# Performance work log

Hardware: AMD Instinct MI355X
Metric: run time of the kernel (lower is better)

The kernel has to match this reference:

```python
import jax, jax.numpy as jnp
import numpy as np

DEPTH = 10
B, F = 8192, 512
NUM_INTERNAL = 2 ** DEPTH - 1   # 1023
NUM_LEAVES = 2 ** DEPTH         # 1024
LEAF_DIMS = 64


def setup_inputs() -> dict:
    key = jax.random.key(0)
    k1, k2, k3 = jax.random.split(key, 3)
    x = jax.random.normal(k1, (B, F), dtype=jnp.float32)
    # All internal-node Dense(1) gates batched into one weight matrix [F, num_internal].
    W = jax.random.normal(k2, (F, NUM_INTERNAL), dtype=jnp.float32) * (1.0 / np.sqrt(F))
    b = jnp.zeros((NUM_INTERNAL,), dtype=jnp.float32)
    leaves_weights = jax.random.normal(k3, (NUM_LEAVES, LEAF_DIMS), dtype=jnp.float32)
    return {"x": x, "W": W, "b": b, "leaves_weights": leaves_weights}


def reference(x, W, b, leaves_weights):
    # All gate probabilities in one fused matmul + sigmoid: [B, num_internal].
    # Node i's gate is column i (BFS / level order, same as the original list of Dense layers).
    p = jax.nn.sigmoid(x @ W + b)
    batch = x.shape[0]
    # Level-by-level probability propagation. prob has shape [B, 2^lvl]:
    # the path probability of each node at the current level.
    prob = jnp.ones((batch, 1), dtype=x.dtype)
    for lvl in range(DEPTH):
        start = 2 ** lvl - 1                      # first node index at this level
        p_lvl = p[:, start:start + 2 ** lvl]      # [B, 2^lvl] gate probs at this level
        # left child gets p * prob, right child gets (1-p) * prob, interleaved in node order
        prob = jnp.stack([p_lvl * prob, (1.0 - p_lvl) * prob], axis=-1)
        prob = prob.reshape(batch, 2 ** (lvl + 1))
    # Leaf-weighted sum: sum_l prob[:, l] * leaves_weights[l, :] -> [B, leaf_dims]
    return prob @ leaves_weights
```

## Files before the change

### kernel.cpp

```cpp
#include <hip/hip_runtime.h>


typedef short bf16x8 __attribute__((ext_vector_type(8)));
typedef float f32x4 __attribute__((ext_vector_type(4)));

#define GLOAD16(g, l) __builtin_amdgcn_global_load_lds( \
    (const __attribute__((address_space(1))) void*)(g), \
    (__attribute__((address_space(3))) void*)(l), 16, 0, 0)

__device__ __forceinline__ unsigned short f2bf(float f) {
    unsigned u = __float_as_uint(f);
    return (unsigned short)((u + 0x7FFFu + ((u >> 16) & 1u)) >> 16);
}

__global__ __launch_bounds__(256) void convert_split(const float* __restrict__ x,
                                                     const float* __restrict__ W,
                                                     unsigned short* __restrict__ xh,
                                                     unsigned short* __restrict__ xl,
                                                     unsigned short* __restrict__ wh,
                                                     unsigned short* __restrict__ wl)
{
    __shared__ float tile[32][33];
    const int b = blockIdx.x;
    const int tid = threadIdx.x;
    if (b < 1024) {
        const float4* xs = reinterpret_cast<const float4*>(x);
        #pragma unroll
        for (int i = 0; i < 4; ++i) {
            const int idx = b * 1024 + i * 256 + tid;
            const float4 v = xs[idx];
            ushort4 h, l;
            h.x = f2bf(v.x); l.x = f2bf(v.x - __uint_as_float((unsigned)h.x << 16));
            h.y = f2bf(v.y); l.y = f2bf(v.y - __uint_as_float((unsigned)h.y << 16));
            h.z = f2bf(v.z); l.z = f2bf(v.z - __uint_as_float((unsigned)h.z << 16));
            h.w = f2bf(v.w); l.w = f2bf(v.w - __uint_as_float((unsigned)h.w << 16));
            reinterpret_cast<ushort4*>(xh)[idx] = h;
            reinterpret_cast<ushort4*>(xl)[idx] = l;
        }
    } else {
        const int tb = b - 1024;
        const int k0 = (tb >> 5) * 32;
        const int n0 = (tb & 31) * 32;
        const int tk = tid >> 5, tn = tid & 31;
        #pragma unroll
        for (int j = 0; j < 4; ++j) {
            const int k = k0 + tk + j * 8;
            const int n = n0 + tn;
            tile[tk + j * 8][tn] = (n < 1023) ? W[(size_t)k * 1023 + n] : 0.f;
        }
        __syncthreads();
        const int wn = tid >> 5, wk = tid & 31;
        #pragma unroll
        for (int j = 0; j < 4; ++j) {
            const int n = n0 + wn + j * 8;
            const float v = tile[wk][wn + j * 8];
            const unsigned short h = f2bf(v);
            const unsigned short lo = f2bf(v - __uint_as_float((unsigned)h << 16));
            wh[(size_t)n * 512 + k0 + wk] = h;
            wl[(size_t)n * 512 + k0 + wk] = lo;
        }
    }
}

__global__ __launch_bounds__(256, 2) void gemm_sig_mfma(
    const unsigned short* __restrict__ xh, const unsigned short* __restrict__ xl,
    const unsigned short* __restrict__ wh, const unsigned short* __restrict__ wl,
    const float* __restrict__ bias, float* __restrict__ p)
{
    __shared__ __align__(16) unsigned short Ah[2][128 * 32];
    __shared__ __align__(16) unsigned short Al[2][128 * 32];
    __shared__ __align__(16) unsigned short Bh[2][128 * 32];
    __shared__ __align__(16) unsigned short Bl[2][128 * 32];

    const int tid = threadIdx.x;
    const int lane = tid & 63;
    const int wv = tid >> 6;
    const int m_base = blockIdx.y * 128;
    const int n_base = blockIdx.x * 128;
    const int wr = wv >> 1, wc = wv & 1;

    f32x4 acc[4][4];
    #pragma unroll
    for (int i = 0; i < 4; ++i)
        #pragma unroll
        for (int j = 0; j < 4; ++j)
            acc[i][j] = (f32x4){0.f, 0.f, 0.f, 0.f};

    const int c0 = tid, c1 = tid + 256;
    const int lb0 = wv * 512;
    const int lb1 = 2048 + wv * 512;
    const int a0row = c0 >> 2, a0kc = (c0 & 3) * 8;
    const int a1row = c1 >> 2, a1kc = (c1 & 3) * 8;
    const int l15 = lane & 15, kg = lane >> 4;

    const size_t ga0 = (size_t)(m_base + a0row) * 512 + a0kc;
    const size_t ga1 = (size_t)(m_base + a1row) * 512 + a1kc;
    const size_t gb0 = (size_t)(n_base + a0row) * 512 + a0kc;
    const size_t gb1 = (size_t)(n_base + a1row) * 512 + a1kc;

    #define STAGE(buf, k0) do { \
        GLOAD16(xh + ga0 + (k0), &Ah[buf][lb0]); \
        GLOAD16(xh + ga1 + (k0), &Ah[buf][lb1]); \
        GLOAD16(xl + ga0 + (k0), &Al[buf][lb0]); \
        GLOAD16(xl + ga1 + (k0), &Al[buf][lb1]); \
        GLOAD16(wh + gb0 + (k0), &Bh[buf][lb0]); \
        GLOAD16(wh + gb1 + (k0), &Bh[buf][lb1]); \
        GLOAD16(wl + gb0 + (k0), &Bl[buf][lb0]); \
        GLOAD16(wl + gb1 + (k0), &Bl[buf][lb1]); \
    } while (0)

    STAGE(0, 0);
    __syncthreads();

    #pragma unroll
    for (int t = 0; t < 16; ++t) {
        const int cur = t & 1;
        if (t < 15) STAGE(cur ^ 1, (t + 1) * 32);

        bf16x8 ah[4], al[4], bh[4], bl[4];
        #pragma unroll
        for (int mi = 0; mi < 4; ++mi) {
            const int off = (wr * 64 + mi * 16 + l15) * 32 + kg * 8;
            ah[mi] = *reinterpret_cast<const bf16x8*>(&Ah[cur][off]);
            al[mi] = *reinterpret_cast<const bf16x8*>(&Al[cur][off]);
        }
        #pragma unroll
        for (int ni = 0; ni < 4; ++ni) {
            const int off = (wc * 64 + ni * 16 + l15) * 32 + kg * 8;
            bh[ni] = *reinterpret_cast<const bf16x8*>(&Bh[cur][off]);
            bl[ni] = *reinterpret_cast<const bf16x8*>(&Bl[cur][off]);
        }
        #pragma unroll
        for (int mi = 0; mi < 4; ++mi)
            #pragma unroll
            for (int ni = 0; ni < 4; ++ni) {
                acc[mi][ni] = __builtin_amdgcn_mfma_f32_16x16x32_bf16(ah[mi], bh[ni], acc[mi][ni], 0, 0, 0);
                acc[mi][ni] = __builtin_amdgcn_mfma_f32_16x16x32_bf16(ah[mi], bl[ni], acc[mi][ni], 0, 0, 0);
                acc[mi][ni] = __builtin_amdgcn_mfma_f32_16x16x32_bf16(al[mi], bh[ni], acc[mi][ni], 0, 0, 0);
            }
        __syncthreads();
    }
    #undef STAGE

    const int l4 = lane >> 4;
    #pragma unroll
    for (int ni = 0; ni < 4; ++ni) {
        const int n = n_base + wc * 64 + ni * 16 + l15;
        if (n < 1023) {
            const float bv = bias[n];
            #pragma unroll
            for (int mi = 0; mi < 4; ++mi) {
                #pragma unroll
                for (int r = 0; r < 4; ++r) {
                    const int m = m_base + wr * 64 + mi * 16 + l4 * 4 + r;
                    const float v = acc[mi][ni][r] + bv;
                    p[(size_t)m * 1024 + 1 + n] = 1.f / (1.f + __expf(-v));
                }
            }
        }
    }
}

__global__ __launch_bounds__(256, 4) void gemm_sig_f32(const float* __restrict__ x,
                                                       const float* __restrict__ W,
                                                       const float* __restrict__ bias,
                                                       float* __restrict__ p)
{
    __shared__ __align__(16) float As[16][128 + 4];
    __shared__ __align__(16) float Bs[16][64 + 4];
    const int tid = threadIdx.x;
    const int m_base = blockIdx.y * 128;
    const int n_base = blockIdx.x * 64;
    const int m0 = (tid >> 4) * 8, n0 = (tid & 15) * 4;
    float acc[8][4];
    #pragma unroll
    for (int i = 0; i < 8; ++i)
        #pragma unroll
        for (int j = 0; j < 4; ++j) acc[i][j] = 0.f;
    const int arow = tid >> 2, acol = (tid & 3) * 4;
    const int bk = tid >> 4, bn = (tid & 15) * 4;
    for (int k0 = 0; k0 < 512; k0 += 16) {
        #pragma unroll
        for (int i = 0; i < 2; ++i) {
            const int row = arow + i * 64;
            const float4 a = *reinterpret_cast<const float4*>(&x[(size_t)(m_base + row) * 512 + k0 + acol]);
            As[0][(acol + 0) * 132 + row] = a.x;
            As[0][(acol + 1) * 132 + row] = a.y;
            As[0][(acol + 2) * 132 + row] = a.z;
            As[0][(acol + 3) * 132 + row] = a.w;
        }
        {
            const int gk = k0 + bk;
            #pragma unroll
            for (int j = 0; j < 4; ++j) {
                const int gn = n_base + bn + j;
                Bs[bk][bn + j] = (gn < 1023) ? W[(size_t)gk * 1023 + gn] : 0.f;
            }
        }
        __syncthreads();
        #pragma unroll
        for (int kk = 0; kk < 16; ++kk) {
            const float4 b4 = *reinterpret_cast<const float4*>(&Bs[kk][n0]);
            const float4 a0 = *reinterpret_cast<const float4*>(&As[kk][m0]);
            const float4 a1 = *reinterpret_cast<const float4*>(&As[kk][m0 + 4]);
            const float a[8] = {a0.x, a0.y, a0.z, a0.w, a1.x, a1.y, a1.z, a1.w};
            const float b[4] = {b4.x, b4.y, b4.z, b4.w};
            #pragma unroll
            for (int i = 0; i < 8; ++i)
                #pragma unroll
                for (int j = 0; j < 4; ++j)
                    acc[i][j] = fmaf(a[i], b[j], acc[i][j]);
        }
        __syncthreads();
    }
    #pragma unroll
    for (int i = 0; i < 8; ++i) {
        const int gm = m_base + m0 + i;
        #pragma unroll
        for (int j = 0; j < 4; ++j) {
            const int gn = n_base + n0 + j;
            if (gn < 1023) {
                float v = acc[i][j] + bias[gn];
                p[(size_t)gm * 1024 + 1 + gn] = 1.0f / (1.0f + __expf(-v));
            }
        }
    }
}

__global__ __launch_bounds__(256, 4) void tree_leaves(const float* __restrict__ p,
                                                      const float* __restrict__ leaves,
                                                      float* __restrict__ out)
{
    __shared__ __align__(16) float prob[8][1024];

    const int tid = threadIdx.x;
    const int row_base = blockIdx.x * 8;
    const int r = tid >> 5, s = tid & 31;
    const float* pr = p + (size_t)(row_base + r) * 1024;

    float prefix = 1.f;
    #pragma unroll
    for (int lvl = 0; lvl < 5; ++lvl) {
        const float v = pr[(1 << lvl) + (s >> (5 - lvl))];
        prefix *= ((s >> (4 - lvl)) & 1) ? (1.f - v) : v;
    }

    float q1[2], q2[4], q3[8], q4[16], q5[32];
    {
        const float v = pr[32 + s];
        q1[0] = prefix * v; q1[1] = prefix * (1.f - v);
    }
    {
        const float2 v2 = *reinterpret_cast<const float2*>(&pr[64 + 2 * s]);
        q2[0] = q1[0] * v2.x; q2[1] = q1[0] * (1.f - v2.x);
        q2[2] = q1[1] * v2.y; q2[3] = q1[1] * (1.f - v2.y);
    }
    {
        const float4 v4 = *reinterpret_cast<const float4*>(&pr[128 + 4 * s]);
        const float v[4] = {v4.x, v4.y, v4.z, v4.w};
        #pragma unroll
        for (int j = 0; j < 4; ++j) {
            q3[2 * j] = q2[j] * v[j]; q3[2 * j + 1] = q2[j] * (1.f - v[j]);
        }
    }
    {
        const float4 va = *reinterpret_cast<const float4*>(&pr[256 + 8 * s]);
        const float4 vb = *reinterpret_cast<const float4*>(&pr[260 + 8 * s]);
        const float v[8] = {va.x, va.y, va.z, va.w, vb.x, vb.y, vb.z, vb.w};
        #pragma unroll
        for (int j = 0; j < 8; ++j) {
            q4[2 * j] = q3[j] * v[j]; q4[2 * j + 1] = q3[j] * (1.f - v[j]);
        }
    }
    {
        float v[16];
        #pragma unroll
        for (int u = 0; u < 4; ++u) {
            const float4 vv = *reinterpret_cast<const float4*>(&pr[512 + 16 * s + 4 * u]);
            v[4 * u] = vv.x; v[4 * u + 1] = vv.y; v[4 * u + 2] = vv.z; v[4 * u + 3] = vv.w;
        }
        #pragma unroll
        for (int j = 0; j < 16; ++j) {
            q5[2 * j] = q4[j] * v[j]; q5[2 * j + 1] = q4[j] * (1.f - v[j]);
        }
    }

    const int sw = (s & 7) << 2;
    #pragma unroll
    for (int u = 0; u < 32; u += 4) {
        float4 q; q.x = q5[u]; q.y = q5[u + 1]; q.z = q5[u + 2]; q.w = q5[u + 3];
        *reinterpret_cast<float4*>(&prob[r][s * 32 + (u ^ sw)]) = q;
    }
    __syncthreads();

    const int cg = tid >> 4, dg = tid & 15;
    float acc[8][4];
    #pragma unroll
    for (int i = 0; i < 8; ++i)
        #pragma unroll
        for (int j = 0; j < 4; ++j) acc[i][j] = 0.f;

    const float* lv_base = leaves + (size_t)(cg * 64) * 64 + dg * 4;
    #pragma unroll 4
    for (int i4 = 0; i4 < 16; ++i4) {
        const int l0 = cg * 64 + i4 * 4;
        const int m_ = (cg * 2 + (i4 >> 3)) & 7;
        const int col = (cg * 64 + ((i4 * 4) ^ (m_ << 2)));
        float4 lv[4];
        #pragma unroll
        for (int j = 0; j < 4; ++j)
            lv[j] = *reinterpret_cast<const float4*>(&leaves[(size_t)(l0 + j) * 64 + dg * 4]);
        #pragma unroll
        for (int rr = 0; rr < 8; ++rr) {
            const float4 pv = *reinterpret_cast<const float4*>(&prob[rr][col]);
            const float pvv[4] = {pv.x, pv.y, pv.z, pv.w};
            #pragma unroll
            for (int j = 0; j < 4; ++j) {
                acc[rr][0] = fmaf(pvv[j], lv[j].x, acc[rr][0]);
                acc[rr][1] = fmaf(pvv[j], lv[j].y, acc[rr][1]);
                acc[rr][2] = fmaf(pvv[j], lv[j].z, acc[rr][2]);
                acc[rr][3] = fmaf(pvv[j], lv[j].w, acc[rr][3]);
            }
        }
    }
    (void)lv_base;

    __syncthreads();
    float* red = &prob[0][0];
    #pragma unroll
    for (int rr = 0; rr < 8; ++rr) {
        float4 q; q.x = acc[rr][0]; q.y = acc[rr][1]; q.z = acc[rr][2]; q.w = acc[rr][3];
        *reinterpret_cast<float4*>(&red[(size_t)(cg * 8 + rr) * 64 + dg * 4]) = q;
    }
    __syncthreads();
    #pragma unroll
    for (int o = tid; o < 512; o += 256) {
        const int rr = o >> 6, d = o & 63;
        float sum = 0.f;
        #pragma unroll
        for (int c = 0; c < 16; ++c)
            sum += red[(size_t)(c * 8 + rr) * 64 + d];
        out[(size_t)(row_base + rr) * 64 + d] = sum;
    }
}

extern "C" void kernel_launch(void* const* d_in, const int* in_sizes, int n_in,
                              void* d_out, int out_size, void* d_ws, size_t ws_size,
                              hipStream_t stream) {
    const float* x      = (const float*)d_in[0];
    const float* W      = (const float*)d_in[1];
    const float* b      = (const float*)d_in[2];
    const float* leaves = (const float*)d_in[3];
    float* out = (float*)d_out;

    float* p = (float*)d_ws;
    const size_t NEED = 52428800;

    if (ws_size >= NEED) {
        unsigned short* xh = (unsigned short*)((char*)d_ws + 33554432);
        unsigned short* xl = (unsigned short*)((char*)d_ws + 41943040);
        unsigned short* wh = (unsigned short*)((char*)d_ws + 50331648);
        unsigned short* wl = (unsigned short*)((char*)d_ws + 51380224);
        convert_split<<<1536, 256, 0, stream>>>(x, W, xh, xl, wh, wl);
        gemm_sig_mfma<<<dim3(8, 64), 256, 0, stream>>>(xh, xl, wh, wl, b, p);
    } else {
        gemm_sig_f32<<<dim3(16, 64), 256, 0, stream>>>(x, W, b, p);
    }
    tree_leaves<<<1024, 256, 0, stream>>>(p, leaves, out);
}
```

Baseline: 129.7 us.

## Switch split-precision GEMM from 3-pass bf16 to 2-pass fp16

Replaces the bf16 hi/lo split (three MFMAs per tile: hh, hl, lh) with fp16. x is kept as a single fp16 value and only W is split into hi/lo, so each tile needs two f16 MFMAs and the xl buffer, its conversion and its loads all go away. The GEMM block grows to 512 threads (8 waves, each computing a 32x64 subtile) with one 16-byte load per thread per operand. The aim is to cut MFMA count, global and LDS traffic, and conversion work, at the cost of accuracy: x now carries only fp16's ~11-bit mantissa, which could matter if the tolerance is tight.

```diff
diff --git a/kernel.cpp b/kernel.cpp
--- a/kernel.cpp
+++ b/kernel.cpp
@@ -1,42 +1,39 @@
 #include <hip/hip_runtime.h>
 
 
-typedef short bf16x8 __attribute__((ext_vector_type(8)));
+typedef _Float16 f16x8 __attribute__((ext_vector_type(8)));
 typedef float f32x4 __attribute__((ext_vector_type(4)));
 
 #define GLOAD16(g, l) __builtin_amdgcn_global_load_lds( \
     (const __attribute__((address_space(1))) void*)(g), \
     (__attribute__((address_space(3))) void*)(l), 16, 0, 0)
 
-__device__ __forceinline__ unsigned short f2bf(float f) {
-    unsigned u = __float_as_uint(f);
-    return (unsigned short)((u + 0x7FFFu + ((u >> 16) & 1u)) >> 16);
-}
-
 __global__ __launch_bounds__(256) void convert_split(const float* __restrict__ x,
                                                      const float* __restrict__ W,
-                                                     unsigned short* __restrict__ xh,
-                                                     unsigned short* __restrict__ xl,
-                                                     unsigned short* __restrict__ wh,
-                                                     unsigned short* __restrict__ wl)
+                                                     _Float16* __restrict__ xh,
+                                                     _Float16* __restrict__ wh,
+                                                     _Float16* __restrict__ wl)
 {
     __shared__ float tile[32][33];
     const int b = blockIdx.x;
     const int tid = threadIdx.x;
     if (b < 1024) {
-        const float4* xs = reinterpret_cast<const float4*>(x);
-        #pragma unroll
-        for (int i = 0; i < 4; ++i) {
-            const int idx = b * 1024 + i * 256 + tid;
-            const float4 v = xs[idx];
-            ushort4 h, l;
-            h.x = f2bf(v.x); l.x = f2bf(v.x - __uint_as_float((unsigned)h.x << 16));
-            h.y = f2bf(v.y); l.y = f2bf(v.y - __uint_as_float((unsigned)h.y << 16));
-            h.z = f2bf(v.z); l.z = f2bf(v.z - __uint_as_float((unsigned)h.z << 16));
-            h.w = f2bf(v.w); l.w = f2bf(v.w - __uint_as_float((unsigned)h.w << 16));
-            reinterpret_cast<ushort4*>(xh)[idx] = h;
-            reinterpret_cast<ushort4*>(xl)[idx] = l;
-        }
+        const int t = b * 256 + tid;
+        const float4* xs = reinterpret_cast<const float4*>(x) + (size_t)t * 4;
+        f16x8 o0, o1;
+        #pragma unroll
+        for (int i = 0; i < 2; ++i) {
+            const float4 v0 = xs[i * 2 + 0];
+            const float4 v1 = xs[i * 2 + 1];
+            f16x8 o;
+            o[0] = (_Float16)v0.x; o[1] = (_Float16)v0.y;
+            o[2] = (_Float16)v0.z; o[3] = (_Float16)v0.w;
+            o[4] = (_Float16)v1.x; o[5] = (_Float16)v1.y;
+            o[6] = (_Float16)v1.z; o[7] = (_Float16)v1.w;
+            if (i == 0) o0 = o; else o1 = o;
+        }
+        reinterpret_cast<f16x8*>(xh)[(size_t)t * 2 + 0] = o0;
+        reinterpret_cast<f16x8*>(xh)[(size_t)t * 2 + 1] = o1;
     } else {
         const int tb = b - 1024;
         const int k0 = (tb >> 5) * 32;
@@ -54,23 +51,22 @@
         for (int j = 0; j < 4; ++j) {
             const int n = n0 + wn + j * 8;
             const float v = tile[wk][wn + j * 8];
-            const unsigned short h = f2bf(v);
-            const unsigned short lo = f2bf(v - __uint_as_float((unsigned)h << 16));
+            const _Float16 h = (_Float16)v;
+            const _Float16 lo = (_Float16)(v - (float)h);
             wh[(size_t)n * 512 + k0 + wk] = h;
             wl[(size_t)n * 512 + k0 + wk] = lo;
         }
     }
 }
 
-__global__ __launch_bounds__(256, 2) void gemm_sig_mfma(
-    const unsigned short* __restrict__ xh, const unsigned short* __restrict__ xl,
-    const unsigned short* __restrict__ wh, const unsigned short* __restrict__ wl,
+__global__ __launch_bounds__(512, 4) void gemm_sig_mfma(
+    const _Float16* __restrict__ xh,
+    const _Float16* __restrict__ wh, const _Float16* __restrict__ wl,
     const float* __restrict__ bias, float* __restrict__ p)
 {
-    __shared__ __align__(16) unsigned short Ah[2][128 * 32];
-    __shared__ __align__(16) unsigned short Al[2][128 * 32];
-    __shared__ __align__(16) unsigned short Bh[2][128 * 32];
-    __shared__ __align__(16) unsigned short Bl[2][128 * 32];
+    __shared__ __align__(16) _Float16 A_[2][128 * 32];
+    __shared__ __align__(16) _Float16 Bh_[2][128 * 32];
+    __shared__ __align__(16) _Float16 Bl_[2][128 * 32];
 
     const int tid = threadIdx.x;
     const int lane = tid & 63;
@@ -79,34 +75,25 @@
     const int n_base = blockIdx.x * 128;
     const int wr = wv >> 1, wc = wv & 1;
 
-    f32x4 acc[4][4];
-    #pragma unroll
-    for (int i = 0; i < 4; ++i)
+    f32x4 acc[2][4];
+    #pragma unroll
+    for (int i = 0; i < 2; ++i)
         #pragma unroll
         for (int j = 0; j < 4; ++j)
             acc[i][j] = (f32x4){0.f, 0.f, 0.f, 0.f};
 
-    const int c0 = tid, c1 = tid + 256;
-    const int lb0 = wv * 512;
-    const int lb1 = 2048 + wv * 512;
-    const int a0row = c0 >> 2, a0kc = (c0 & 3) * 8;
-    const int a1row = c1 >> 2, a1kc = (c1 & 3) * 8;
+    const int row = tid >> 2;
+    const int oct = (tid & 3) * 8;
+    const int lb = wv * 512;
+    const size_t ga = (size_t)(m_base + row) * 512 + oct;
+    const size_t gb = (size_t)(n_base + row) * 512 + oct;
+
     const int l15 = lane & 15, kg = lane >> 4;
 
-    const size_t ga0 = (size_t)(m_base + a0row) * 512 + a0kc;
-    const size_t ga1 = (size_t)(m_base + a1row) * 512 + a1kc;
-    const size_t gb0 = (size_t)(n_base + a0row) * 512 + a0kc;
-    const size_t gb1 = (size_t)(n_base + a1row) * 512 + a1kc;
-
     #define STAGE(buf, k0) do { \
-        GLOAD16(xh + ga0 + (k0), &Ah[buf][lb0]); \
-        GLOAD16(xh + ga1 + (k0), &Ah[buf][lb1]); \
-        GLOAD16(xl + ga0 + (k0), &Al[buf][lb0]); \
-        GLOAD16(xl + ga1 + (k0), &Al[buf][lb1]); \
-        GLOAD16(wh + gb0 + (k0), &Bh[buf][lb0]); \
-        GLOAD16(wh + gb1 + (k0), &Bh[buf][lb1]); \
-        GLOAD16(wl + gb0 + (k0), &Bl[buf][lb0]); \
-        GLOAD16(wl + gb1 + (k0), &Bl[buf][lb1]); \
+        GLOAD16(xh + ga + (k0), &A_[buf][lb]);  \
+        GLOAD16(wh + gb + (k0), &Bh_[buf][lb]); \
+        GLOAD16(wl + gb + (k0), &Bl_[buf][lb]); \
     } while (0)
 
     STAGE(0, 0);
@@ -117,26 +104,24 @@
         const int cur = t & 1;
         if (t < 15) STAGE(cur ^ 1, (t + 1) * 32);
 
-        bf16x8 ah[4], al[4], bh[4], bl[4];
-        #pragma unroll
-        for (int mi = 0; mi < 4; ++mi) {
-            const int off = (wr * 64 + mi * 16 + l15) * 32 + kg * 8;
-            ah[mi] = *reinterpret_cast<const bf16x8*>(&Ah[cur][off]);
-            al[mi] = *reinterpret_cast<const bf16x8*>(&Al[cur][off]);
+        f16x8 a_[2], bh_[4], bl_[4];
+        #pragma unroll
+        for (int mi = 0; mi < 2; ++mi) {
+            const int off = (wr * 32 + mi * 16 + l15) * 32 + kg * 8;
+            a_[mi] = *reinterpret_cast<const f16x8*>(&A_[cur][off]);
         }
         #pragma unroll
         for (int ni = 0; ni < 4; ++ni) {
             const int off = (wc * 64 + ni * 16 + l15) * 32 + kg * 8;
-            bh[ni] = *reinterpret_cast<const bf16x8*>(&Bh[cur][off]);
-            bl[ni] = *reinterpret_cast<const bf16x8*>(&Bl[cur][off]);
-        }
-        #pragma unroll
-        for (int mi = 0; mi < 4; ++mi)
+            bh_[ni] = *reinterpret_cast<const f16x8*>(&Bh_[cur][off]);
+            bl_[ni] = *reinterpret_cast<const f16x8*>(&Bl_[cur][off]);
+        }
+        #pragma unroll
+        for (int mi = 0; mi < 2; ++mi)
             #pragma unroll
             for (int ni = 0; ni < 4; ++ni) {
-                acc[mi][ni] = __builtin_amdgcn_mfma_f32_16x16x32_bf16(ah[mi], bh[ni], acc[mi][ni], 0, 0, 0);
-                acc[mi][ni] = __builtin_amdgcn_mfma_f32_16x16x32_bf16(ah[mi], bl[ni], acc[mi][ni], 0, 0, 0);
-                acc[mi][ni] = __builtin_amdgcn_mfma_f32_16x16x32_bf16(al[mi], bh[ni], acc[mi][ni], 0, 0, 0);
+                acc[mi][ni] = __builtin_amdgcn_mfma_f32_16x16x32_f16(a_[mi], bh_[ni], acc[mi][ni], 0, 0, 0);
+                acc[mi][ni] = __builtin_amdgcn_mfma_f32_16x16x32_f16(a_[mi], bl_[ni], acc[mi][ni], 0, 0, 0);
             }
         __syncthreads();
     }
@@ -149,10 +134,10 @@
         if (n < 1023) {
             const float bv = bias[n];
             #pragma unroll
-            for (int mi = 0; mi < 4; ++mi) {
+            for (int mi = 0; mi < 2; ++mi) {
                 #pragma unroll
                 for (int r = 0; r < 4; ++r) {
-                    const int m = m_base + wr * 64 + mi * 16 + l4 * 4 + r;
+                    const int m = m_base + wr * 32 + mi * 16 + l4 * 4 + r;
                     const float v = acc[mi][ni][r] + bv;
                     p[(size_t)m * 1024 + 1 + n] = 1.f / (1.f + __expf(-v));
                 }
@@ -300,7 +285,6 @@
         #pragma unroll
         for (int j = 0; j < 4; ++j) acc[i][j] = 0.f;
 
-    const float* lv_base = leaves + (size_t)(cg * 64) * 64 + dg * 4;
     #pragma unroll 4
     for (int i4 = 0; i4 < 16; ++i4) {
         const int l0 = cg * 64 + i4 * 4;
@@ -323,7 +307,6 @@
             }
         }
     }
-    (void)lv_base;
 
     __syncthreads();
     float* red = &prob[0][0];
@@ -354,15 +337,14 @@
     float* out = (float*)d_out;
 
     float* p = (float*)d_ws;
-    const size_t NEED = 52428800;
+    const size_t NEED = 44040192;
 
     if (ws_size >= NEED) {
-        unsigned short* xh = (unsigned short*)((char*)d_ws + 33554432);
-        unsigned short* xl = (unsigned short*)((char*)d_ws + 41943040);
-        unsigned short* wh = (unsigned short*)((char*)d_ws + 50331648);
-        unsigned short* wl = (unsigned short*)((char*)d_ws + 51380224);
-        convert_split<<<1536, 256, 0, stream>>>(x, W, xh, xl, wh, wl);
-        gemm_sig_mfma<<<dim3(8, 64), 256, 0, stream>>>(xh, xl, wh, wl, b, p);
+        _Float16* xh = (_Float16*)((char*)d_ws + 33554432);
+        _Float16* wh = (_Float16*)((char*)d_ws + 41943040);
+        _Float16* wl = (_Float16*)((char*)d_ws + 42991616);
+        convert_split<<<1536, 256, 0, stream>>>(x, W, xh, wh, wl);
+        gemm_sig_mfma<<<dim3(8, 64), 512, 0, stream>>>(xh, wh, wl, b, p);
     } else {
         gemm_sig_f32<<<dim3(16, 64), 256, 0, stream>>>(x, W, b, p);
     }
```

Measured after the change: 118.9 us. 8.3% less time.
